# Performance work log

Hardware: AMD Instinct MI355X
Metric: run time of the kernel (lower is better)

## Reference

```python
import jax, jax.numpy as jnp
import numpy as np

N = 8192
IN_F = 512
OUT_F = 512
ALPHA = 0.2
NEG_BIG = -9.0e15


def setup_inputs() -> dict:
    key = jax.random.key(0)
    k1, k2, k3, k4 = jax.random.split(key, 4)
    adjacency = jax.random.randint(k1, (N, N), 0, 2, dtype=jnp.int32)
    features = jax.random.normal(k2, (N, IN_F), dtype=jnp.float32)
    # Linear weight stored as [in, out] (h = x @ W)
    W = jax.random.normal(k3, (IN_F, OUT_F), dtype=jnp.float32) * (1.0 / np.sqrt(IN_F))
    attn = jax.random.normal(k4, (2 * OUT_F, 1), dtype=jnp.float32) * 0.05
    return {"adjacency": adjacency, "features": features, "W": W, "attn": attn}


def reference(adjacency, features, W, attn):
    h = features @ W  # [N, F]
    # Additive decomposition of concat([h_i, h_j]) @ attn:
    # score_ij = a1 . h_i + a2 . h_j  (identical math, no NxNx2F tensor)
    a1 = attn[:OUT_F, 0]  # [F]
    a2 = attn[OUT_F:, 0]  # [F]
    s1 = h @ a1  # [N] contribution of source node i
    s2 = h @ a2  # [N] contribution of target node j
    e = jax.nn.leaky_relu(s1[:, None] + s2[None, :], negative_slope=ALPHA)  # [N, N]
    e = jnp.where(adjacency > 0, e, NEG_BIG)
    attention = jax.nn.softmax(e, axis=1)  # [N, N]
    h_prime = attention @ h  # [N, F]
    return jax.nn.elu(h_prime)
```

## Files before the change

kernel.cpp:

```cpp
#include <hip/hip_runtime.h>
#include <hip/hip_bf16.h>
#include <cstdint>

#define NN 8192
#define F 512
#define LOG2E 1.4426950408889634f

typedef __attribute__((ext_vector_type(8))) short bf16x8;
typedef __attribute__((ext_vector_type(4))) float f32x4;
typedef unsigned int uint32;
typedef unsigned long long u64;
typedef unsigned char uchar;

__device__ __forceinline__ short f2bf(float x){
  __hip_bfloat16 h = __float2bfloat16(x);
  return *reinterpret_cast<short*>(&h);
}

__global__ __launch_bounds__(256) void k_wa(const float* __restrict__ W, const float* __restrict__ attn,
                     float* __restrict__ wa){
  const int lane = threadIdx.x&63, wid = threadIdx.x>>6;
  const int id = blockIdx.x*4 + wid;
  const int b = id>>9, c = id&511;
  const float4* Wr = (const float4*)(W + (size_t)c*F);
  const float4* av = (const float4*)(attn + b*F);
  float s = 0.f;
  #pragma unroll
  for (int h=0;h<2;++h){
    const int k = lane + h*64;
    const float4 wv = Wr[k], a = av[k];
    s += wv.x*a.x + wv.y*a.y + wv.z*a.z + wv.w*a.w;
  }
  for (int off=32;off;off>>=1) s += __shfl_down(s,off);
  if (lane==0) wa[id] = s;
}

__global__ __launch_bounds__(256) void k_tw(const float* __restrict__ W, short* __restrict__ WbT){
  __shared__ short t[64][72];
  const int k0 = blockIdx.x*64, n0 = blockIdx.y*64;
  #pragma unroll
  for (int it=0;it<16;++it){
    const int idx = it*256 + threadIdx.x;
    const int r = idx>>6, c = idx&63;
    t[r][c] = f2bf(W[(size_t)(k0+r)*F + n0 + c]);
  }
  __syncthreads();
  #pragma unroll
  for (int it=0;it<2;++it){
    const int idx = it*256 + threadIdx.x;
    const int n = idx>>3, g = idx&7;
    short v[8];
    #pragma unroll
    for (int e=0;e<8;++e) v[e] = t[g*8+e][n];
    *(uint4*)(WbT + (size_t)(n0+n)*F + k0 + g*8) = *(const uint4*)v;
  }
}

__global__ __launch_bounds__(256) void k_prep(const float* __restrict__ X, const float* __restrict__ wa,
    short* __restrict__ Xb, float2* __restrict__ rowAB, uint32* __restrict__ uwb){
  const int lane = threadIdx.x&63, wid = threadIdx.x>>6;
  const int row = blockIdx.x*4 + wid;
  const float4* X4 = (const float4*)(X + (size_t)row*F);
  const float4* A4 = (const float4*)wa;
  const float4* B4 = (const float4*)(wa + F);
  uint2* Xb4 = (uint2*)(Xb + (size_t)row*F);
  float a1 = 0.f, a2 = 0.f;
  #pragma unroll
  for (int h=0;h<2;++h){
    const int c = lane + h*64;
    const float4 x = X4[c];
    const float4 a = A4[c];
    const float4 b = B4[c];
    a1 += x.x*a.x + x.y*a.y + x.z*a.z + x.w*a.w;
    a2 += x.x*b.x + x.y*b.y + x.z*b.z + x.w*b.w;
    short o[4] = {f2bf(x.x),f2bf(x.y),f2bf(x.z),f2bf(x.w)};
    Xb4[c] = *(const uint2*)o;
  }
  for (int off=32;off;off>>=1){ a1 += __shfl_down(a1,off); a2 += __shfl_down(a2,off); }
  if (lane==0){
    const float s1 = a1*LOG2E, s2 = a2*LOG2E;
    rowAB[row] = make_float2(exp2f(s1), exp2f(0.2f*s1));
    const float u = exp2f(s2), w = exp2f(0.2f*s2);
    uwb[row] = (uint32)(unsigned short)f2bf(u) | ((uint32)(unsigned short)f2bf(w)<<16);
  }
}

__global__ __launch_bounds__(256,2) void k_gemm1(const short* __restrict__ Xb,
    const short* __restrict__ WbT, short* __restrict__ HT){
  __shared__ char smem[33280];
  short* At = (short*)smem;
  short* Bt = (short*)(smem + 16384);
  const int tid=threadIdx.x, lane=tid&63, wid=tid>>6;
  const int m0 = blockIdx.x*128, n0 = blockIdx.y*128;
  f32x4 acc[2][8];
  #pragma unroll
  for (int a=0;a<2;++a)
    #pragma unroll
    for (int b=0;b<8;++b) acc[a][b] = (f32x4){0.f,0.f,0.f,0.f};

  for (int t=0;t<8;++t){
    const int k0 = t*64;
    __syncthreads();
    #pragma unroll
    for (int rnd=0;rnd<4;++rnd){
      const int s = rnd*256 + tid;
      const int n = s>>3, kc = s&7;
      uint4 va = *(const uint4*)(Xb  + (size_t)(m0+n)*F + k0 + kc*8);
      uint4 vb = *(const uint4*)(WbT + (size_t)(n0+n)*F + k0 + kc*8);
      const int off = n*128 + ((kc^(n&7))*16);
      *(uint4*)((char*)At + off) = va;
      *(uint4*)((char*)Bt + off) = vb;
    }
    __syncthreads();
    #pragma unroll
    for (int ks=0;ks<2;++ks){
      const int kc = ks*4 + (lane>>4);
      int r0 = wid*32 + (lane&15);
      int r1 = r0 + 16;
      bf16x8 af0 = *(const bf16x8*)((char*)At + r0*128 + ((kc^(r0&7))*16));
      bf16x8 af1 = *(const bf16x8*)((char*)At + r1*128 + ((kc^(r1&7))*16));
      #pragma unroll
      for (int nf=0;nf<8;++nf){
        const int c = nf*16 + (lane&15);
        bf16x8 bf = *(const bf16x8*)((char*)Bt + c*128 + ((kc^(c&7))*16));
        acc[0][nf] = __builtin_amdgcn_mfma_f32_16x16x32_bf16(af0, bf, acc[0][nf],0,0,0);
        acc[1][nf] = __builtin_amdgcn_mfma_f32_16x16x32_bf16(af1, bf, acc[1][nf],0,0,0);
      }
    }
  }
  __syncthreads();
  short* ct = (short*)smem;
  #pragma unroll
  for (int mf=0;mf<2;++mf)
    #pragma unroll
    for (int nf=0;nf<8;++nf)
      #pragma unroll
      for (int q=0;q<4;++q){
        int r = wid*32 + mf*16 + (lane>>4)*4 + q;
        int c = nf*16 + (lane&15);
        ct[r*130+c] = f2bf(acc[mf][nf][q]);
      }
  __syncthreads();
  {
    const int c = tid>>1, ih0 = (tid&1)*64;
    #pragma unroll
    for (int i8=0;i8<8;++i8){
      short v[8];
      #pragma unroll
      for (int e=0;e<8;++e) v[e] = ct[(ih0+i8*8+e)*130 + c];
      *(uint4*)(HT + (size_t)(n0+c)*NN + m0 + ih0 + i8*8) = *(const uint4*)v;
    }
  }
}

__global__ __launch_bounds__(256,2) void k_pv(const int* __restrict__ adj,
    const short* __restrict__ HT, const uint32* __restrict__ uwb,
    const float2* __restrict__ rowAB, float* __restrict__ Zp,
    float* __restrict__ P0, float* __restrict__ P1,
    float* __restrict__ P2, float* __restrict__ P3, int ksteps, int KS){
  __shared__ short Bt2[2][512*32];
  __shared__ short At2[2][64*32];
  __shared__ uint32 uwl[2048];
  const int tid=threadIdx.x, lane=tid&63, wid=tid>>6;
  int mx, kz;
  if (KS == 4){
    const int id = blockIdx.x;
    kz = (id&7)>>1;
    mx = ((id>>3)<<1) + (id&1);
  } else { kz = 0; mx = blockIdx.x; }
  const int m0 = mx*64;
  const int kz0 = kz*(ksteps*32);
  float* const outs[4] = {P0,P1,P2,P3};
  float* outP = outs[kz];

  {
    const uint4* src = (const uint4*)(uwb + kz0);
    uint4 v0 = src[tid], v1 = src[256+tid];
    ((uint4*)uwl)[tid] = v0; ((uint4*)uwl)[256+tid] = v1;
  }

  const int kcs = (tid&3) ^ ((tid>>3)&3);
  const short* gB = HT + (size_t)(tid>>2)*NN + kz0 + kcs*8;

  const int ar = tid>>2, aq = tid&3;
  const float2 E = rowAB[m0 + ar];
  const float A0 = E.x, B0c = E.y;
  const int* adjp = adj + (size_t)(m0+ar)*NN + kz0 + aq*8;
  const int aoff = ar*64 + ((aq ^ ((ar>>1)&3))<<4);

  const int bofs = (((lane>>4) ^ ((lane>>1)&3))<<4);
  const int l15_64 = (lane&15)*64;

  f32x4 acc[4][8];
  #pragma unroll
  for (int i=0;i<4;++i)
    #pragma unroll
    for (int j=0;j<8;++j) acc[i][j] = (f32x4){0.f,0.f,0.f,0.f};
  float zacc = 0.f;

  uint4 b0,b1,b2,b3,b4,b5,b6,b7;
  int4  aA0,aA1, aB0,aB1;

#define PV_BLOAD(tt) { \
    const short* g = gB + (size_t)(tt)*32; \
    b0 = *(const uint4*)(g);               b1 = *(const uint4*)(g + (size_t)1*64*NN); \
    b2 = *(const uint4*)(g + (size_t)2*64*NN); b3 = *(const uint4*)(g + (size_t)3*64*NN); \
    b4 = *(const uint4*)(g + (size_t)4*64*NN); b5 = *(const uint4*)(g + (size_t)5*64*NN); \
    b6 = *(const uint4*)(g + (size_t)6*64*NN); b7 = *(const uint4*)(g + (size_t)7*64*NN); }

#define PV_BWRITE(buf) { \
    uint4* d = (uint4*)(Bt2[buf]); \
    d[      tid] = b0; d[ 256+tid] = b1; d[ 512+tid] = b2; d[ 768+tid] = b3; \
    d[1024+tid] = b4; d[1280+tid] = b5; d[1536+tid] = b6; d[1792+tid] = b7; }

#define PV_ALOAD(r0v,r1v,tt) { \
    r0v = *(const int4*)(adjp + (size_t)(tt)*32); \
    r1v = *(const int4*)(adjp + (size_t)(tt)*32 + 4); }

#define PV_AGEN(abuf, r0v, r1v, tt) { \
    const uint32* uwt = &uwl[(tt)*32 + aq*8]; \
    const uint4 u0 = *(const uint4*)uwt; \
    const uint4 u1 = *(const uint4*)(uwt+4); \
    const uint32 pk[8] = {u0.x,u0.y,u0.z,u0.w,u1.x,u1.y,u1.z,u1.w}; \
    const int    aa[8] = {r0v.x,r0v.y,r0v.z,r0v.w,r1v.x,r1v.y,r1v.z,r1v.w}; \
    short av[8]; \
    _Pragma("unroll") \
    for (int e=0;e<8;++e){ \
      const float u = __uint_as_float(pk[e]<<16); \
      const float w = __uint_as_float(pk[e]&0xffff0000u); \
      float v = fmaxf(A0*u, B0c*w); \
      v = (aa[e] > 0) ? v : 0.f; \
      zacc += v; \
      av[e] = f2bf(v); } \
    *(uint4*)((char*)(At2[abuf]) + aoff) = *(const uint4*)av; }

#define PV_MFMA(buf) { \
    bf16x8 af[4]; \
    _Pragma("unroll") \
    for (int mf=0;mf<4;++mf) \
      af[mf] = *(const bf16x8*)((char*)(At2[buf]) + mf*1024 + l15_64 + bofs); \
    _Pragma("unroll") \
    for (int nf=0;nf<8;++nf){ \
      const bf16x8 bv = *(const bf16x8*)((char*)(Bt2[buf]) + wid*8192 + nf*1024 + l15_64 + bofs); \
      _Pragma("unroll") \
      for (int mf=0;mf<4;++mf) \
        acc[mf][nf] = __builtin_amdgcn_mfma_f32_16x16x32_bf16(af[mf], bv, acc[mf][nf],0,0,0); } }

  PV_ALOAD(aA0,aA1, 0);
  PV_BLOAD(0);
  __syncthreads();
  PV_AGEN(0, aA0,aA1, 0);
  PV_BWRITE(0);
  PV_ALOAD(aB0,aB1, 1);
  __syncthreads();

  for (int t=0; t<ksteps; t+=2){
    {
      if (t+1 < ksteps) PV_BLOAD(t+1);
      if (t+2 < ksteps) PV_ALOAD(aA0,aA1, t+2);
      PV_MFMA(0);
      if (t+1 < ksteps){ PV_AGEN(1, aB0,aB1, t+1); PV_BWRITE(1); }
      __syncthreads();
    }
    if (t+1 < ksteps){
      if (t+2 < ksteps) PV_BLOAD(t+2);
      if (t+3 < ksteps) PV_ALOAD(aB0,aB1, t+3);
      PV_MFMA(1);
      if (t+2 < ksteps){ PV_AGEN(0, aA0,aA1, t+2); PV_BWRITE(0); }
      __syncthreads();
    }
  }

  zacc += __shfl_xor(zacc, 1);
  zacc += __shfl_xor(zacc, 2);
  if (aq == 0) Zp[(size_t)kz*NN + m0 + ar] = zacc;
  #pragma unroll
  for (int mf=0;mf<4;++mf)
    #pragma unroll
    for (int nf=0;nf<8;++nf){
      const int col = wid*128 + nf*16 + (lane&15);
      #pragma unroll
      for (int qq=0;qq<4;++qq){
        const int row = m0 + mf*16 + (lane>>4)*4 + qq;
        outP[(size_t)row*F + col] = acc[mf][nf][qq];
      }
    }
#undef PV_BLOAD
#undef PV_BWRITE
#undef PV_ALOAD
#undef PV_AGEN
#undef PV_MFMA
}

__global__ __launch_bounds__(256) void k_red(const float* __restrict__ P1,
    const float* __restrict__ P2, const float* __restrict__ P3,
    const float* __restrict__ Zp, float* __restrict__ out, int ks){
  const size_t i = ((size_t)blockIdx.x*256 + threadIdx.x)*4;
  const int row = (int)(i >> 9);
  float4 a = *(float4*)(out+i);
  float Z = Zp[row];
  if (ks > 1){
    Z += Zp[NN+row] + Zp[2*NN+row] + Zp[3*NN+row];
    const float4 b1 = *(const float4*)(P1+i);
    const float4 b2 = *(const float4*)(P2+i);
    const float4 b3 = *(const float4*)(P3+i);
    a.x += b1.x+b2.x+b3.x; a.y += b1.y+b2.y+b3.y;
    a.z += b1.z+b2.z+b3.z; a.w += b1.w+b2.w+b3.w;
  }
  const float s = 1.f/Z;
  a.x*=s; a.y*=s; a.z*=s; a.w*=s;
  a.x = (a.x>0.f)?a.x:expm1f(a.x);
  a.y = (a.y>0.f)?a.y:expm1f(a.y);
  a.z = (a.z>0.f)?a.z:expm1f(a.z);
  a.w = (a.w>0.f)?a.w:expm1f(a.w);
  *(float4*)(out+i) = a;
}

extern "C" void kernel_launch(void* const* d_in, const int* in_sizes, int n_in,
                              void* d_out, int out_size, void* d_ws, size_t ws_size,
                              hipStream_t stream) {
  (void)in_sizes; (void)n_in; (void)out_size;
  const int*   adj  = (const int*)d_in[0];
  const float* X    = (const float*)d_in[1];
  const float* W    = (const float*)d_in[2];
  const float* attn = (const float*)d_in[3];
  float* out = (float*)d_out;
  char* ws = (char*)d_ws;
  short*  HT   = (short*)(ws);
  short*  Xb   = (short*)(ws + 8388608);
  short*  WbT  = (short*)(ws + 16777216);
  uint32* uwb  = (uint32*)(ws + 17301504);
  float2* rowAB= (float2*)(ws + 17334272);
  float*  wa   = (float*)(ws + 17399808);
  float*  Zp   = (float*)(ws + 17403904);
  float*  P1   = (float*)(ws + 17534976);
  float*  P2   = (float*)(ws + 34312192);
  float*  P3   = (float*)(ws + 51089408);
  const int KS = (ws_size >= 67866624ull) ? 4 : 1;
  const int ksteps = 256/KS;

  k_wa   <<<dim3(256),    dim3(256), 0, stream>>>(W, attn, wa);
  k_tw   <<<dim3(8,8),    dim3(256), 0, stream>>>(W, WbT);
  k_prep <<<dim3(2048),   dim3(256), 0, stream>>>(X, wa, Xb, rowAB, uwb);
  k_gemm1<<<dim3(64,4),   dim3(256), 0, stream>>>(Xb, WbT, HT);
  k_pv   <<<dim3(128*KS), dim3(256), 0, stream>>>(adj, HT, uwb, rowAB, Zp, out, P1, P2, P3, ksteps, KS);
  k_red  <<<dim3(4096),   dim3(256), 0, stream>>>(P1, P2, P3, Zp, out, KS);
}
```

Before: 180.1 us.

## Use single-buffered 64-wide K tiles with XOR swizzle in attention-PV kernel

The fused attention-times-H kernel changes from double-buffered 32-wide K tiles to a single shared buffer holding 64-wide K tiles, with an 8-way XOR swizzle on both the A and B tiles. This halves the number of K-step iterations and their barriers and doubles the MFMA work per synchronization, but global loads for the next tile now overlap only with the current MFMA phase instead of running through a ping-pong buffer. LDS size stays about the same, and the B tile load is split into two halves to bound register pressure.

```diff
diff --git a/kernel.cpp b/kernel.cpp
--- a/kernel.cpp
+++ b/kernel.cpp
@@ -158,8 +158,8 @@
     const float2* __restrict__ rowAB, float* __restrict__ Zp,
     float* __restrict__ P0, float* __restrict__ P1,
     float* __restrict__ P2, float* __restrict__ P3, int ksteps, int KS){
-  __shared__ short Bt2[2][512*32];
-  __shared__ short At2[2][64*32];
+  __shared__ short Bt[512*64];
+  __shared__ short At[64*64];
   __shared__ uint32 uwl[2048];
   const int tid=threadIdx.x, lane=tid&63, wid=tid>>6;
   int mx, kz;
@@ -169,7 +169,7 @@
     mx = ((id>>3)<<1) + (id&1);
   } else { kz = 0; mx = blockIdx.x; }
   const int m0 = mx*64;
-  const int kz0 = kz*(ksteps*32);
+  const int kz0 = kz*(ksteps*64);
   float* const outs[4] = {P0,P1,P2,P3};
   float* outP = outs[kz];
 
@@ -179,17 +179,15 @@
     ((uint4*)uwl)[tid] = v0; ((uint4*)uwl)[256+tid] = v1;
   }
 
-  const int kcs = (tid&3) ^ ((tid>>3)&3);
-  const short* gB = HT + (size_t)(tid>>2)*NN + kz0 + kcs*8;
+  const int kcs = (tid&7) ^ ((tid>>3)&7);
+  const short* gBa = HT + (size_t)(tid>>3)*NN + kz0 + kcs*8;
 
   const int ar = tid>>2, aq = tid&3;
   const float2 E = rowAB[m0 + ar];
   const float A0 = E.x, B0c = E.y;
   const int* adjp = adj + (size_t)(m0+ar)*NN + kz0 + aq*8;
-  const int aoff = ar*64 + ((aq ^ ((ar>>1)&3))<<4);
-
-  const int bofs = (((lane>>4) ^ ((lane>>1)&3))<<4);
-  const int l15_64 = (lane&15)*64;
+  const int aoff0 = ar*128 + (((aq  ) ^ (ar&7))*16);
+  const int aoff1 = ar*128 + (((aq+4) ^ (ar&7))*16);
 
   f32x4 acc[4][8];
   #pragma unroll
@@ -201,24 +199,24 @@
   uint4 b0,b1,b2,b3,b4,b5,b6,b7;
   int4  aA0,aA1, aB0,aB1;
 
-#define PV_BLOAD(tt) { \
-    const short* g = gB + (size_t)(tt)*32; \
-    b0 = *(const uint4*)(g);               b1 = *(const uint4*)(g + (size_t)1*64*NN); \
-    b2 = *(const uint4*)(g + (size_t)2*64*NN); b3 = *(const uint4*)(g + (size_t)3*64*NN); \
-    b4 = *(const uint4*)(g + (size_t)4*64*NN); b5 = *(const uint4*)(g + (size_t)5*64*NN); \
-    b6 = *(const uint4*)(g + (size_t)6*64*NN); b7 = *(const uint4*)(g + (size_t)7*64*NN); }
-
-#define PV_BWRITE(buf) { \
-    uint4* d = (uint4*)(Bt2[buf]); \
+#define PV_BLOAD_H(h, tt) { \
+    const short* g = gBa + (size_t)(h)*256*NN + (size_t)(tt)*64; \
+    b0 = *(const uint4*)(g);                   b1 = *(const uint4*)(g + (size_t)1*32*NN); \
+    b2 = *(const uint4*)(g + (size_t)2*32*NN); b3 = *(const uint4*)(g + (size_t)3*32*NN); \
+    b4 = *(const uint4*)(g + (size_t)4*32*NN); b5 = *(const uint4*)(g + (size_t)5*32*NN); \
+    b6 = *(const uint4*)(g + (size_t)6*32*NN); b7 = *(const uint4*)(g + (size_t)7*32*NN); }
+
+#define PV_BWRITE_H(h) { \
+    uint4* d = (uint4*)Bt + (h)*2048; \
     d[      tid] = b0; d[ 256+tid] = b1; d[ 512+tid] = b2; d[ 768+tid] = b3; \
     d[1024+tid] = b4; d[1280+tid] = b5; d[1536+tid] = b6; d[1792+tid] = b7; }
 
-#define PV_ALOAD(r0v,r1v,tt) { \
-    r0v = *(const int4*)(adjp + (size_t)(tt)*32); \
-    r1v = *(const int4*)(adjp + (size_t)(tt)*32 + 4); }
-
-#define PV_AGEN(abuf, r0v, r1v, tt) { \
-    const uint32* uwt = &uwl[(tt)*32 + aq*8]; \
+#define PV_ALOAD(r0v,r1v,h,tt) { \
+    r0v = *(const int4*)(adjp + (size_t)(tt)*64 + (h)*32); \
+    r1v = *(const int4*)(adjp + (size_t)(tt)*64 + (h)*32 + 4); }
+
+#define PV_AGEN(aoffv, r0v, r1v, h, tt) { \
+    const uint32* uwt = &uwl[(tt)*64 + (h)*32 + aq*8]; \
     const uint4 u0 = *(const uint4*)uwt; \
     const uint4 u1 = *(const uint4*)(uwt+4); \
     const uint32 pk[8] = {u0.x,u0.y,u0.z,u0.w,u1.x,u1.y,u1.z,u1.w}; \
@@ -232,41 +230,50 @@
       v = (aa[e] > 0) ? v : 0.f; \
       zacc += v; \
       av[e] = f2bf(v); } \
-    *(uint4*)((char*)(At2[abuf]) + aoff) = *(const uint4*)av; }
-
-#define PV_MFMA(buf) { \
-    bf16x8 af[4]; \
+    *(uint4*)((char*)At + (aoffv)) = *(const uint4*)av; }
+
+#define PV_MFMA64() { \
     _Pragma("unroll") \
-    for (int mf=0;mf<4;++mf) \
-      af[mf] = *(const bf16x8*)((char*)(At2[buf]) + mf*1024 + l15_64 + bofs); \
-    _Pragma("unroll") \
-    for (int nf=0;nf<8;++nf){ \
-      const bf16x8 bv = *(const bf16x8*)((char*)(Bt2[buf]) + wid*8192 + nf*1024 + l15_64 + bofs); \
+    for (int ks=0;ks<2;++ks){ \
+      const int kc = ks*4 + (lane>>4); \
+      bf16x8 af[4]; \
       _Pragma("unroll") \
-      for (int mf=0;mf<4;++mf) \
-        acc[mf][nf] = __builtin_amdgcn_mfma_f32_16x16x32_bf16(af[mf], bv, acc[mf][nf],0,0,0); } }
-
-  PV_ALOAD(aA0,aA1, 0);
-  PV_BLOAD(0);
-  __syncthreads();
-  PV_AGEN(0, aA0,aA1, 0);
-  PV_BWRITE(0);
-  PV_ALOAD(aB0,aB1, 1);
-  __syncthreads();
-
-  for (int t=0; t<ksteps; t+=2){
-    {
-      if (t+1 < ksteps) PV_BLOAD(t+1);
-      if (t+2 < ksteps) PV_ALOAD(aA0,aA1, t+2);
-      PV_MFMA(0);
-      if (t+1 < ksteps){ PV_AGEN(1, aB0,aB1, t+1); PV_BWRITE(1); }
-      __syncthreads();
-    }
+      for (int mf=0;mf<4;++mf){ \
+        const int r = mf*16 + (lane&15); \
+        af[mf] = *(const bf16x8*)((char*)At + r*128 + ((kc^(r&7))*16)); } \
+      _Pragma("unroll") \
+      for (int nf=0;nf<8;++nf){ \
+        const int c = wid*128 + nf*16 + (lane&15); \
+        const bf16x8 bv = *(const bf16x8*)((char*)Bt + c*128 + ((kc^(c&7))*16)); \
+        _Pragma("unroll") \
+        for (int mf=0;mf<4;++mf) \
+          acc[mf][nf] = __builtin_amdgcn_mfma_f32_16x16x32_bf16(af[mf], bv, acc[mf][nf],0,0,0); } } }
+
+  PV_ALOAD(aA0,aA1, 0, 0);
+  PV_ALOAD(aB0,aB1, 1, 0);
+  PV_BLOAD_H(0, 0);
+  __syncthreads();
+  PV_BWRITE_H(0);
+  PV_AGEN(aoff0, aA0,aA1, 0, 0);
+  PV_BLOAD_H(1, 0);
+  PV_AGEN(aoff1, aB0,aB1, 1, 0);
+  PV_BWRITE_H(1);
+  __syncthreads();
+
+  for (int t=0; t<ksteps; ++t){
     if (t+1 < ksteps){
-      if (t+2 < ksteps) PV_BLOAD(t+2);
-      if (t+3 < ksteps) PV_ALOAD(aB0,aB1, t+3);
-      PV_MFMA(1);
-      if (t+2 < ksteps){ PV_AGEN(0, aA0,aA1, t+2); PV_BWRITE(0); }
+      PV_BLOAD_H(0, t+1);
+      PV_ALOAD(aA0,aA1, 0, t+1);
+      PV_ALOAD(aB0,aB1, 1, t+1);
+    }
+    PV_MFMA64();
+    __syncthreads();
+    if (t+1 < ksteps){
+      PV_BWRITE_H(0);
+      PV_AGEN(aoff0, aA0,aA1, 0, t+1);
+      PV_BLOAD_H(1, t+1);
+      PV_AGEN(aoff1, aB0,aB1, 1, t+1);
+      PV_BWRITE_H(1);
       __syncthreads();
     }
   }
@@ -285,11 +292,11 @@
         outP[(size_t)row*F + col] = acc[mf][nf][qq];
       }
     }
-#undef PV_BLOAD
-#undef PV_BWRITE
+#undef PV_BLOAD_H
+#undef PV_BWRITE_H
 #undef PV_ALOAD
 #undef PV_AGEN
-#undef PV_MFMA
+#undef PV_MFMA64
 }
 
 __global__ __launch_bounds__(256) void k_red(const float* __restrict__ P1,
@@ -337,7 +344,7 @@
   float*  P2   = (float*)(ws + 34312192);
   float*  P3   = (float*)(ws + 51089408);
   const int KS = (ws_size >= 67866624ull) ? 4 : 1;
-  const int ksteps = 256/KS;
+  const int ksteps = 128/KS;
 
   k_wa   <<<dim3(256),    dim3(256), 0, stream>>>(W, attn, wa);
   k_tw   <<<dim3(8,8),    dim3(256), 0, stream>>>(W, WbT);
```

New measurement: 152.4 us (median of 2 runs). 15.4% less time.
